# Kernel optimization log

Measured on AMD Instinct MI355X. Metric: run time of the kernel, lower is better.

## Reference

```python
import jax, jax.numpy as jnp
import numpy as np

N_KERNELS = 21
N_LAYERS = 2
N_HEADS = 8
ATT_DIM = 32
FF_HID = 100
EMB = 300


def kernel_mus(n):
    mus = [1.0]
    bin_size = 2.0 / (n - 1)
    mus.append(1.0 - bin_size / 2.0)
    for _ in range(1, n - 1):
        mus.append(mus[-1] - bin_size)
    return np.array(mus, dtype=np.float32)


def kernel_sigmas(n):
    return np.array([0.001] + [0.1] * (n - 1), dtype=np.float32)


def setup_inputs() -> dict:
    key = jax.random.key(0)
    ks = jax.random.split(key, 12)
    B, LQ, LD = 32, 64, 512
    u = lambda k, s, a: jax.random.uniform(k, s, jnp.float32, -a, a)
    return dict(
        q_embed=jax.random.normal(ks[0], (B, LQ, EMB), jnp.float32),
        d_embed=jax.random.normal(ks[1], (B, LD, EMB), jnp.float32),
        mask_q=(jax.random.uniform(ks[2], (B, LQ)) > 0.1).astype(jnp.float32),
        mask_d=(jax.random.uniform(ks[3], (B, LD)) > 0.1).astype(jnp.float32),
        mixer=jnp.full((1, 1, 1), 0.5, jnp.float32),
        nn_scaler=jnp.full((1,), 0.01, jnp.float32),
        ff_w1=u(ks[4], (N_LAYERS, EMB, FF_HID), 0.05),
        ff_b1=jnp.zeros((N_LAYERS, FF_HID), jnp.float32),
        ff_w2=u(ks[5], (N_LAYERS, FF_HID, EMB), 0.05),
        ff_b2=jnp.zeros((N_LAYERS, EMB), jnp.float32),
        ln1_g=jnp.ones((N_LAYERS, EMB), jnp.float32),
        ln1_b=jnp.zeros((N_LAYERS, EMB), jnp.float32),
        att_w=u(ks[6], (N_LAYERS, EMB, 3 * ATT_DIM), 0.05),
        att_b=jnp.zeros((N_LAYERS, 3 * ATT_DIM), jnp.float32),
        out_w=u(ks[7], (N_LAYERS, ATT_DIM, EMB), 0.05),
        out_b=jnp.zeros((N_LAYERS, EMB), jnp.float32),
        ln2_g=jnp.ones((N_LAYERS, EMB), jnp.float32),
        ln2_b=jnp.zeros((N_LAYERS, EMB), jnp.float32),
        dense_w=u(ks[8], (1, N_KERNELS), 0.014),
    )


def _layer_norm(x, g, b, eps=1e-6):
    m = jnp.mean(x, -1, keepdims=True)
    s = jnp.std(x, -1, keepdims=True, ddof=1)  # torch std is unbiased
    return g * (x - m) / (s + eps) + b


def _encoder(x, mask, p):
    # AllenNLP StackedSelfAttentionEncoder: [FF -> res+LN -> MHSA -> res+LN] x2
    B, T, E = x.shape
    scale = jnp.sqrt(jnp.float32(E // N_HEADS))
    hd = ATT_DIM // N_HEADS
    for l in range(N_LAYERS):
        h = jax.nn.relu(x @ p['ff_w1'][l] + p['ff_b1'][l]) @ p['ff_w2'][l] + p['ff_b2'][l]
        h = _layer_norm(h + x, p['ln1_g'][l], p['ln1_b'][l])
        c = h @ p['att_w'][l] + p['att_b'][l]              # [B,T,3*ATT_DIM]
        q = c[..., :ATT_DIM].reshape(B, T, N_HEADS, hd)
        k = c[..., ATT_DIM:2 * ATT_DIM].reshape(B, T, N_HEADS, hd)
        v = c[..., 2 * ATT_DIM:].reshape(B, T, N_HEADS, hd)
        sims = jnp.einsum('bqhd,bkhd->bhqk', q / scale, k)
        m = mask[:, None, None, :]
        att = jax.nn.softmax(sims * m, axis=-1) * m         # AllenNLP masked_softmax
        att = att / (jnp.sum(att, -1, keepdims=True) + 1e-13)
        o = jnp.einsum('bhqk,bkhd->bqhd', att, v).reshape(B, T, ATT_DIM)
        o = o @ p['out_w'][l] + p['out_b'][l]
        x = _layer_norm(o + h, p['ln2_g'][l], p['ln2_b'][l])
    return x


def reference(q_embed, d_embed, mask_q, mask_d, mixer, nn_scaler,
              ff_w1, ff_b1, ff_w2, ff_b2, ln1_g, ln1_b,
              att_w, att_b, out_w, out_b, ln2_g, ln2_b, dense_w):
    p = dict(ff_w1=ff_w1, ff_b1=ff_b1, ff_w2=ff_w2, ff_b2=ff_b2,
             ln1_g=ln1_g, ln1_b=ln1_b, att_w=att_w, att_b=att_b,
             out_w=out_w, out_b=out_b, ln2_g=ln2_g, ln2_b=ln2_b)
    mu = jnp.asarray(kernel_mus(N_KERNELS))        # [K]
    sigma = jnp.asarray(kernel_sigmas(N_KERNELS))  # [K]
    mq = mask_q[..., None]
    md = mask_d[..., None]
    q = q_embed * mq
    d = d_embed * md
    qc = _encoder(q, mask_q, p)
    dc = _encoder(d, mask_d, p)
    q = (mixer * q + (1.0 - mixer) * qc) * mq
    d = (mixer * d + (1.0 - mixer) * dc) * md
    qd_mask = mask_q[:, :, None] * mask_d[:, None, :]  # [B,Q,D]
    qn = q / (jnp.linalg.norm(q, axis=-1, keepdims=True) + 1e-13)
    dn = d / (jnp.linalg.norm(d, axis=-1, keepdims=True) + 1e-13)
    cos = jnp.einsum('bqe,bde->bqd', qn, dn) * qd_mask
    # Gaussian RBF soft histogram: [B,Q,D,K]
    kr = jnp.exp(-(cos[..., None] - mu) ** 2 / (2.0 * sigma ** 2)) * qd_mask[..., None]
    pkq = jnp.sum(kr, axis=2)                                 # [B,Q,K]
    log_pkq = jnp.log2(jnp.clip(pkq, 1e-10)) * nn_scaler
    per_kernel = jnp.sum(log_pkq * mq, axis=1)                # [B,K]
    return jnp.squeeze(per_kernel @ dense_w.T, axis=1)        # [B]
```

## Files before the change

kernel.cpp:

```cpp
#include <hip/hip_runtime.h>
#include <hip/hip_bf16.h>

#define BATCH 32
#define LQ 64
#define LD 512
#define EMB 300
#define FFH 100
#define ATTD 32
#define NH 8
#define NK 21
#define MQ (BATCH * LQ)
#define MD (BATCH * LD)
#define MALL (MQ + MD)

typedef __attribute__((ext_vector_type(8))) short bf16x8;
typedef __attribute__((ext_vector_type(4))) float f32x4;

__device__ __forceinline__ float wave_sum(float v) {
    #pragma unroll
    for (int off = 32; off > 0; off >>= 1) v += __shfl_xor(v, off);
    return v;
}

__device__ __forceinline__ float bf2f(__hip_bfloat16 h) {
    return __bfloat162float(h);
}

__device__ __forceinline__ float4 bf4_to_f4(const __hip_bfloat16* p) {
    uint2 u = *(const uint2*)p;
    float4 f;
    f.x = __uint_as_float((u.x & 0xffffu) << 16);
    f.y = __uint_as_float(u.x & 0xffff0000u);
    f.z = __uint_as_float((u.y & 0xffffu) << 16);
    f.w = __uint_as_float(u.y & 0xffff0000u);
    return f;
}

__global__ void maskmul_all(const float* __restrict__ q_embed, const float* __restrict__ d_embed,
                            const float* __restrict__ mask_q, const float* __restrict__ mask_d,
                            __hip_bfloat16* __restrict__ xbf, float* __restrict__ mall) {
    int i = blockIdx.x * blockDim.x + threadIdx.x;
    if (i >= MALL * EMB) return;
    int tok = i / EMB;
    float m, v;
    if (tok < MQ) {
        m = mask_q[tok];
        v = q_embed[i];
    } else {
        m = mask_d[tok - MQ];
        v = d_embed[i - MQ * EMB];
    }
    xbf[i] = __float2bfloat16(v * m);
    if (i % EMB == 0) mall[tok] = m;
}

__device__ __forceinline__ void conv_seg(const float* __restrict__ w, __hip_bfloat16* __restrict__ wt,
                                         int j, int K, int N) {
    int l = j / (K * N);
    int r = j % (K * N);
    int k = r / N, n = r % N;
    wt[(size_t)l * N * K + (size_t)n * K + k] = __float2bfloat16(w[j]);
}
__global__ void convert_all(const float* __restrict__ w1, const float* __restrict__ w2,
                            const float* __restrict__ aw, const float* __restrict__ ow,
                            __hip_bfloat16* __restrict__ w1t, __hip_bfloat16* __restrict__ w2t,
                            __hip_bfloat16* __restrict__ awt, __hip_bfloat16* __restrict__ owt) {
    int i = blockIdx.x * blockDim.x + threadIdx.x;
    const int S1 = 2 * EMB * FFH;
    const int S2 = S1 + 2 * 320 * 128;
    const int S3 = S2 + 2 * EMB * 96;
    const int S4 = S3 + 2 * 320 * 32;
    if (i < S1) {
        conv_seg(w1, w1t, i, EMB, FFH);
    } else if (i < S2) {
        int j = i - S1;
        int l = j / (320 * 128);
        int r = j % (320 * 128);
        int n = r / 128, k = r % 128;
        float v = (n < EMB && k < FFH) ? w2[(size_t)l * FFH * EMB + (size_t)k * EMB + n] : 0.f;
        w2t[j] = __float2bfloat16(v);
    } else if (i < S3) {
        conv_seg(aw, awt, i - S2, EMB, 96);
    } else if (i < S4) {
        int j = i - S3;
        int l = j / (320 * 32);
        int r = j % (320 * 32);
        int n = r / 32, k = r % 32;
        float v = (n < EMB && k < ATTD) ? ow[(size_t)l * ATTD * EMB + (size_t)k * EMB + n] : 0.f;
        owt[j] = __float2bfloat16(v);
    }
}

__device__ __forceinline__ void stage_row8(const __hip_bfloat16* __restrict__ src, bool rowvalid,
                                           int K, int gk, __hip_bfloat16* dst) {
    if (rowvalid && gk + 8 <= K) {
        const uint2* p = (const uint2*)(src + gk);
        uint2 a = p[0], b = p[1];
        *(uint2*)dst = a;
        *(uint2*)(dst + 4) = b;
    } else {
        #pragma unroll
        for (int j = 0; j < 8; j++)
            dst[j] = (rowvalid && gk + j < K) ? src[gk + j] : __float2bfloat16(0.f);
    }
}

template <bool RELU>
__global__ __launch_bounds__(256) void gemm_mfma(const __hip_bfloat16* __restrict__ A,
                                                 const __hip_bfloat16* __restrict__ Bt,
                                                 const float* __restrict__ bias,
                                                 __hip_bfloat16* __restrict__ Cb,
                                                 int M, int Nr, int Ns, int K) {
    __shared__ __align__(16) __hip_bfloat16 As[64][40];
    __shared__ __align__(16) __hip_bfloat16 Bs[64][40];
    const int tid = threadIdx.x;
    const int m0 = blockIdx.y * 64, n0 = blockIdx.x * 64;
    const int lane = tid & 63;
    const int wv = tid >> 6;
    const int wm = wv >> 1, wn = wv & 1;
    const int l15 = lane & 15, lg = lane >> 4;
    const int srow = tid >> 2, sk8 = (tid & 3) * 8;
    f32x4 acc[2][2] = {};
    const int NS = (K + 31) >> 5;
    const __hip_bfloat16* arow = A + (size_t)(m0 + srow) * K;
    const bool bvalid = (n0 + srow) < Nr;
    const __hip_bfloat16* brow = Bt + (size_t)(n0 + srow) * K;

    for (int s = 0; s < NS; s++) {
        const int gk = (s << 5) + sk8;
        if (s) __syncthreads();
        stage_row8(arow, true, K, gk, &As[srow][sk8]);
        stage_row8(brow, bvalid, K, gk, &Bs[srow][sk8]);
        __syncthreads();
        bf16x8 af0 = *(const bf16x8*)&As[wm * 32 + l15][lg * 8];
        bf16x8 af1 = *(const bf16x8*)&As[wm * 32 + 16 + l15][lg * 8];
        bf16x8 bf0 = *(const bf16x8*)&Bs[wn * 32 + l15][lg * 8];
        bf16x8 bf1 = *(const bf16x8*)&Bs[wn * 32 + 16 + l15][lg * 8];
        acc[0][0] = __builtin_amdgcn_mfma_f32_16x16x32_bf16(af0, bf0, acc[0][0], 0, 0, 0);
        acc[0][1] = __builtin_amdgcn_mfma_f32_16x16x32_bf16(af0, bf1, acc[0][1], 0, 0, 0);
        acc[1][0] = __builtin_amdgcn_mfma_f32_16x16x32_bf16(af1, bf0, acc[1][0], 0, 0, 0);
        acc[1][1] = __builtin_amdgcn_mfma_f32_16x16x32_bf16(af1, bf1, acc[1][1], 0, 0, 0);
    }

    #pragma unroll
    for (int fc = 0; fc < 2; fc++) {
        int col = n0 + wn * 32 + fc * 16 + l15;
        if (col >= Ns) continue;
        float bs = (col < Nr) ? bias[col] : 0.f;
        #pragma unroll
        for (int fr = 0; fr < 2; fr++) {
            int rbase = m0 + wm * 32 + fr * 16 + lg * 4;
            #pragma unroll
            for (int r = 0; r < 4; r++) {
                float v = acc[fr][fc][r] + bs;
                if (RELU) v = fmaxf(v, 0.f);
                Cb[(size_t)(rbase + r) * Ns + col] = __float2bfloat16(v);
            }
        }
    }
}

template <int NSTEP, int KSTR, int ASTR>
__global__ __launch_bounds__(256) void gemm_ln_direct(const __hip_bfloat16* __restrict__ A,
                                                      const __hip_bfloat16* __restrict__ Bt,
                                                      const float* __restrict__ bias,
                                                      const __hip_bfloat16* __restrict__ Res,
                                                      const float* __restrict__ g,
                                                      const float* __restrict__ beta,
                                                      __hip_bfloat16* __restrict__ Y) {
    const int tid = threadIdx.x;
    const int wv = tid >> 6;
    const int lane = tid & 63;
    const int l15 = lane & 15, lg = lane >> 4;
    const int m0 = blockIdx.x * 64 + wv * 16;

    f32x4 acc[19];
    #pragma unroll
    for (int fc = 0; fc < 19; fc++) acc[fc] = (f32x4){0.f, 0.f, 0.f, 0.f};

    #pragma unroll
    for (int ks = 0; ks < NSTEP; ks++) {
        const int kb = ks * 32 + lg * 8;
        bf16x8 af = *(const bf16x8*)(A + (size_t)(m0 + l15) * ASTR + kb);
        #pragma unroll
        for (int fc = 0; fc < 19; fc++) {
            bf16x8 bf = *(const bf16x8*)(Bt + (size_t)(fc * 16 + l15) * KSTR + kb);
            acc[fc] = __builtin_amdgcn_mfma_f32_16x16x32_bf16(af, bf, acc[fc], 0, 0, 0);
        }
    }

    float rs[4] = {0.f, 0.f, 0.f, 0.f};
    #pragma unroll
    for (int fc = 0; fc < 19; fc++) {
        int col = fc * 16 + l15;
        bool valid = col < EMB;
        float bs = valid ? bias[col] : 0.f;
        #pragma unroll
        for (int r = 0; r < 4; r++) {
            float v = 0.f;
            if (valid) v = acc[fc][r] + bs + bf2f(Res[(size_t)(m0 + lg * 4 + r) * EMB + col]);
            acc[fc][r] = v;
            rs[r] += v;
        }
    }
    #pragma unroll
    for (int r = 0; r < 4; r++)
        #pragma unroll
        for (int off = 1; off < 16; off <<= 1)
            rs[r] += __shfl_xor(rs[r], off);
    float mean[4], invv[4];
    #pragma unroll
    for (int r = 0; r < 4; r++) mean[r] = rs[r] * (1.f / EMB);

    float rq[4] = {0.f, 0.f, 0.f, 0.f};
    #pragma unroll
    for (int fc = 0; fc < 19; fc++) {
        int col = fc * 16 + l15;
        if (col < EMB) {
            #pragma unroll
            for (int r = 0; r < 4; r++) {
                float d = acc[fc][r] - mean[r];
                rq[r] += d * d;
            }
        }
    }
    #pragma unroll
    for (int r = 0; r < 4; r++) {
        #pragma unroll
        for (int off = 1; off < 16; off <<= 1)
            rq[r] += __shfl_xor(rq[r], off);
        float stdv = sqrtf(rq[r] * (1.f / (EMB - 1)));
        invv[r] = 1.f / (stdv + 1e-6f);
    }
    #pragma unroll
    for (int fc = 0; fc < 19; fc++) {
        int col = fc * 16 + l15;
        if (col >= EMB) continue;
        float gv = g[col], bv = beta[col];
        #pragma unroll
        for (int r = 0; r < 4; r++) {
            float y = gv * (acc[fc][r] - mean[r]) * invv[r] + bv;
            Y[(size_t)(m0 + lg * 4 + r) * EMB + col] = __float2bfloat16(y);
        }
    }
}

__global__ __launch_bounds__(256) void cos_mfma(const __hip_bfloat16* __restrict__ Qn,
                                                const __hip_bfloat16* __restrict__ Dn,
                                                float* __restrict__ Cos) {
    __shared__ __align__(16) __hip_bfloat16 As[64][40];
    __shared__ __align__(16) __hip_bfloat16 Bs[64][40];
    const int b = blockIdx.y;
    const int n0 = blockIdx.x * 64;
    const int tid = threadIdx.x;
    const int lane = tid & 63;
    const int wv = tid >> 6;
    const int wm = wv >> 1, wn = wv & 1;
    const int l15 = lane & 15, lg = lane >> 4;
    const int srow = tid >> 2, sk8 = (tid & 3) * 8;
    f32x4 acc[2][2] = {};
    const int NS = (EMB + 31) >> 5;
    const __hip_bfloat16* arow = Qn + ((size_t)b * LQ + srow) * EMB;
    const __hip_bfloat16* brow = Dn + ((size_t)b * LD + n0 + srow) * EMB;

    for (int s = 0; s < NS; s++) {
        const int gk = (s << 5) + sk8;
        if (s) __syncthreads();
        stage_row8(arow, true, EMB, gk, &As[srow][sk8]);
        stage_row8(brow, true, EMB, gk, &Bs[srow][sk8]);
        __syncthreads();
        bf16x8 af0 = *(const bf16x8*)&As[wm * 32 + l15][lg * 8];
        bf16x8 af1 = *(const bf16x8*)&As[wm * 32 + 16 + l15][lg * 8];
        bf16x8 bf0 = *(const bf16x8*)&Bs[wn * 32 + l15][lg * 8];
        bf16x8 bf1 = *(const bf16x8*)&Bs[wn * 32 + 16 + l15][lg * 8];
        acc[0][0] = __builtin_amdgcn_mfma_f32_16x16x32_bf16(af0, bf0, acc[0][0], 0, 0, 0);
        acc[0][1] = __builtin_amdgcn_mfma_f32_16x16x32_bf16(af0, bf1, acc[0][1], 0, 0, 0);
        acc[1][0] = __builtin_amdgcn_mfma_f32_16x16x32_bf16(af1, bf0, acc[1][0], 0, 0, 0);
        acc[1][1] = __builtin_amdgcn_mfma_f32_16x16x32_bf16(af1, bf1, acc[1][1], 0, 0, 0);
    }

    float* cb = Cos + (size_t)b * LQ * LD;
    #pragma unroll
    for (int fc = 0; fc < 2; fc++) {
        int col = n0 + wn * 32 + fc * 16 + l15;
        #pragma unroll
        for (int fr = 0; fr < 2; fr++) {
            int rbase = wm * 32 + fr * 16 + lg * 4;
            #pragma unroll
            for (int r = 0; r < 4; r++) {
                cb[(size_t)(rbase + r) * LD + col] = acc[fr][fc][r];
            }
        }
    }
}

template <int T, int RPB, int KS>
__device__ __forceinline__ void attn_body(const __hip_bfloat16* __restrict__ cseg,
                                          const float* __restrict__ mask,
                                          __hip_bfloat16* __restrict__ oseg,
                                          int bh, int rb, char* smem) {
    constexpr int BLK = 512;
    float4* Ks = (float4*)smem;
    float4* Vs = Ks + T;
    float* part = (float*)(Vs + T);
    float* nmask_s = part + RPB * 5 * (KS - 1);
    const int b = bh / NH, h = bh % NH;
    const int tid = threadIdx.x;
    const __hip_bfloat16* base = cseg + (size_t)b * T * 96;

    if (tid == 0) *nmask_s = 0.f;
    __syncthreads();
    float lnm = 0.f;
    for (int j = tid; j < T; j += BLK) {
        float m = mask[b * T + j];
        float4 kv = bf4_to_f4(base + (size_t)j * 96 + ATTD + h * 4);
        float4 vv = bf4_to_f4(base + (size_t)j * 96 + 2 * ATTD + h * 4);
        kv.x *= m; kv.y *= m; kv.z *= m; kv.w *= m;
        vv.x *= m; vv.y *= m; vv.z *= m; vv.w *= m;
        Ks[j] = kv;
        Vs[j] = vv;
        lnm += 1.f - m;
    }
    lnm = wave_sum(lnm);
    if ((tid & 63) == 0 && lnm != 0.f) atomicAdd(nmask_s, lnm);
    __syncthreads();

    const int r = rb * RPB + (tid % RPB);
    const int ks = tid / RPB;
    const float inv_scale = 0.16439898730535729f;
    float4 qv = bf4_to_f4(base + (size_t)r * 96 + h * 4);
    qv.x *= inv_scale; qv.y *= inv_scale; qv.z *= inv_scale; qv.w *= inv_scale;

    float Sall = 0.f, ox = 0.f, oy = 0.f, oz = 0.f, ow = 0.f;
    constexpr int KC = T / KS;
    const int k0 = ks * KC;
    #pragma unroll 4
    for (int k = k0; k < k0 + KC; k++) {
        float4 kv = Ks[k];
        float4 vv = Vs[k];
        float s = fmaf(qv.x, kv.x, fmaf(qv.y, kv.y, fmaf(qv.z, kv.z, qv.w * kv.w)));
        float e = __expf(s);
        Sall += e;
        ox = fmaf(e, vv.x, ox);
        oy = fmaf(e, vv.y, oy);
        oz = fmaf(e, vv.z, oz);
        ow = fmaf(e, vv.w, ow);
    }
    if (ks > 0) {
        float* p = &part[((ks - 1) * RPB + (tid % RPB)) * 5];
        p[0] = Sall; p[1] = ox; p[2] = oy; p[3] = oz; p[4] = ow;
    }
    __syncthreads();
    if (ks == 0) {
        #pragma unroll
        for (int s2 = 0; s2 < KS - 1; s2++) {
            const float* p = &part[(s2 * RPB + r - rb * RPB) * 5];
            Sall += p[0]; ox += p[1]; oy += p[2]; oz += p[3]; ow += p[4];
        }
        float Sm = Sall - *nmask_s;
        float inv = 1.f / (Sm + 1e-13f * Sall);
        __hip_bfloat16* op = oseg + (size_t)(b * T + r) * ATTD + h * 4;
        op[0] = __float2bfloat16(ox * inv);
        op[1] = __float2bfloat16(oy * inv);
        op[2] = __float2bfloat16(oz * inv);
        op[3] = __float2bfloat16(ow * inv);
    }
}

__global__ __launch_bounds__(512) void attn_both(const __hip_bfloat16* __restrict__ cbf,
                                                 const float* __restrict__ mask_q,
                                                 const float* __restrict__ mask_d,
                                                 __hip_bfloat16* __restrict__ o32) {
    __shared__ __align__(16) char smem[24576];
    int blk = blockIdx.x;
    if (blk < BATCH * NH) {
        attn_body<LQ, 64, 8>(cbf, mask_q, o32, blk, 0, smem);
    } else {
        int bid = blk - BATCH * NH;
        attn_body<LD, 128, 4>(cbf + (size_t)MQ * 96, mask_d, o32 + (size_t)MQ * ATTD,
                              bid >> 2, bid & 3, smem);
    }
}

__global__ __launch_bounds__(256) void mixnorm_bf(const __hip_bfloat16* __restrict__ x,
                                                  const __hip_bfloat16* __restrict__ xc,
                                                  const float* __restrict__ mask,
                                                  const float* __restrict__ mixer,
                                                  __hip_bfloat16* __restrict__ out) {
    int wid = (blockIdx.x * 256 + threadIdx.x) >> 6;
    int lane = threadIdx.x & 63;
    float mixv = mixer[0];
    float mval = mask[wid];
    const __hip_bfloat16* xr = x + (size_t)wid * EMB;
    const __hip_bfloat16* xcr = xc + (size_t)wid * EMB;
    float v[5];
    float s2 = 0.f;
    #pragma unroll
    for (int r = 0; r < 5; r++) {
        int idx = lane + r * 64;
        float val = 0.f;
        if (idx < EMB) val = (mixv * bf2f(xr[idx]) + (1.f - mixv) * bf2f(xcr[idx])) * mval;
        v[r] = val;
        s2 += val * val;
    }
    s2 = wave_sum(s2);
    float inv = 1.f / (sqrtf(s2) + 1e-13f);
    __hip_bfloat16* o = out + (size_t)wid * EMB;
    #pragma unroll
    for (int r = 0; r < 5; r++) {
        int idx = lane + r * 64;
        if (idx < EMB) o[idx] = __float2bfloat16(v[r] * inv);
    }
}

__global__ __launch_bounds__(256) void pool_kernel(const float* __restrict__ Cos,
                                                   const float* __restrict__ mask_q,
                                                   const float* __restrict__ mask_d,
                                                   const float* __restrict__ nn_scaler,
                                                   float* __restrict__ lp) {
    int wid = (blockIdx.x * 256 + threadIdx.x) >> 6;
    int lane = threadIdx.x & 63;
    int b = wid >> 6, qi = wid & 63;
    const float* crow = Cos + ((size_t)b * LQ + qi) * LD;
    const float* md = mask_d + b * LD;
    float acc[NK];
    #pragma unroll
    for (int k = 0; k < NK; k++) acc[k] = 0.f;
    #pragma unroll
    for (int rr = 0; rr < LD / 64; rr++) {
        int dj = rr * 64 + lane;
        float m = md[dj];
        if (m != 0.f) {
            float cv = crow[dj];
            float d0 = cv - 1.0f;
            acc[0] += __expf(d0 * d0 * -500000.0f);
            #pragma unroll
            for (int g = 0; g < 4; g++) {
                float mu_a = 0.95f - 0.5f * g;
                float dc = cv - mu_a;
                float t = __expf(dc * dc * -50.0f);
                float r = __expf(fmaf(-10.0f, dc, -0.5f));
                #pragma unroll
                for (int j = 0; j < 5; j++) {
                    acc[1 + 5 * g + j] += t;
                    t *= r;
                    r *= 0.36787944117144233f;
                }
            }
        }
    }
    float mq = mask_q[b * LQ + qi];
    float ns = nn_scaler[0];
    #pragma unroll
    for (int k = 0; k < NK; k++) {
        float s = wave_sum(acc[k]);
        if (lane == 0) lp[((size_t)b * LQ + qi) * NK + k] = log2f(fmaxf(s, 1e-10f)) * ns * mq;
    }
}

__global__ void final_kernel(const float* __restrict__ lp, const float* __restrict__ dense_w,
                             float* __restrict__ out) {
    int b = blockIdx.x;
    int t = threadIdx.x;
    float s = 0.f;
    if (t < NK) {
        for (int qi = 0; qi < LQ; qi++) s += lp[((size_t)b * LQ + qi) * NK + t];
        s *= dense_w[t];
    }
    s = wave_sum(s);
    if (t == 0) out[b] = s;
}

extern "C" void kernel_launch(void* const* d_in, const int* in_sizes, int n_in,
                              void* d_out, int out_size, void* d_ws, size_t ws_size,
                              hipStream_t stream) {
    (void)in_sizes; (void)n_in; (void)out_size; (void)ws_size;
    const float* q_embed  = (const float*)d_in[0];
    const float* d_embed  = (const float*)d_in[1];
    const float* mask_q   = (const float*)d_in[2];
    const float* mask_d   = (const float*)d_in[3];
    const float* mixer    = (const float*)d_in[4];
    const float* nn_scaler= (const float*)d_in[5];
    const float* ff_w1    = (const float*)d_in[6];
    const float* ff_b1    = (const float*)d_in[7];
    const float* ff_w2    = (const float*)d_in[8];
    const float* ff_b2    = (const float*)d_in[9];
    const float* ln1_g    = (const float*)d_in[10];
    const float* ln1_b    = (const float*)d_in[11];
    const float* att_w    = (const float*)d_in[12];
    const float* att_b    = (const float*)d_in[13];
    const float* out_w    = (const float*)d_in[14];
    const float* out_b    = (const float*)d_in[15];
    const float* ln2_g    = (const float*)d_in[16];
    const float* ln2_b    = (const float*)d_in[17];
    const float* dense_w  = (const float*)d_in[18];
    float* out = (float*)d_out;

    float* ws   = (float*)d_ws;
    float* cosb = ws;
    float* lp   = cosb + 1048576;
    float* mall = lp + 43008;
    __hip_bfloat16* xbf   = (__hip_bfloat16*)(mall + MALL);
    __hip_bfloat16* xcbf  = xbf  + (size_t)MALL * EMB;
    __hip_bfloat16* xc2bf = xcbf + (size_t)MALL * EMB;
    __hip_bfloat16* hbf   = xc2bf + (size_t)MALL * EMB;
    __hip_bfloat16* t1bf  = hbf  + (size_t)MALL * EMB;
    __hip_bfloat16* cbf   = t1bf + (size_t)MALL * 128;
    __hip_bfloat16* o32bf = cbf  + (size_t)MALL * 96;
    __hip_bfloat16* w1t   = o32bf + (size_t)MALL * ATTD;
    __hip_bfloat16* w2t   = w1t + 2 * FFH * EMB;
    __hip_bfloat16* awt   = w2t + 2 * 320 * 128;
    __hip_bfloat16* owt   = awt + 2 * 96 * EMB;

    convert_all<<<(220000 + 255) / 256, 256, 0, stream>>>(ff_w1, ff_w2, att_w, out_w,
                                                          w1t, w2t, awt, owt);
    maskmul_all<<<(MALL * EMB + 255) / 256, 256, 0, stream>>>(q_embed, d_embed, mask_q, mask_d,
                                                              xbf, mall);

    const __hip_bfloat16* xcur = xbf;
    for (int l = 0; l < 2; l++) {
        __hip_bfloat16* xout = (l == 0) ? xcbf : xc2bf;
        gemm_mfma<true><<<dim3(2, MALL / 64), 256, 0, stream>>>(
            xcur, w1t + (size_t)l * FFH * EMB, ff_b1 + l * FFH, t1bf, MALL, FFH, 128, EMB);
        gemm_ln_direct<4, 128, 128><<<MALL / 64, 256, 0, stream>>>(
            t1bf, w2t + (size_t)l * 320 * 128, ff_b2 + l * EMB, xcur,
            ln1_g + l * EMB, ln1_b + l * EMB, hbf);
        gemm_mfma<false><<<dim3(2, MALL / 64), 256, 0, stream>>>(
            hbf, awt + (size_t)l * 96 * EMB, att_b + l * 96, cbf, MALL, 96, 96, EMB);
        attn_both<<<BATCH * NH + BATCH * NH * (LD / 128), 512, 0, stream>>>(
            cbf, mask_q, mask_d, o32bf);
        gemm_ln_direct<1, 32, 32><<<MALL / 64, 256, 0, stream>>>(
            o32bf, owt + (size_t)l * 320 * 32, out_b + l * EMB, hbf,
            ln2_g + l * EMB, ln2_b + l * EMB, xout);
        xcur = xout;
    }

    mixnorm_bf<<<MALL / 4, 256, 0, stream>>>(xbf, xc2bf, mall, mixer, hbf);

    cos_mfma<<<dim3(LD / 64, BATCH), 256, 0, stream>>>(hbf, hbf + (size_t)MQ * EMB, cosb);

    pool_kernel<<<(BATCH * LQ) / 4, 256, 0, stream>>>(cosb, mask_q, mask_d, nn_scaler, lp);

    final_kernel<<<BATCH, 64, 0, stream>>>(lp, dense_w, out);
}
```

Measured before the change: 243.0 us.

## Fuse RBF kernel pooling into cosine MFMA epilogue with atomic accumulation

The cosine-similarity GEMM now computes the Gaussian RBF soft histogram directly in its epilogue. It reduces across lanes and atomically adds per-query kernel sums into a buffer that is zeroed in the weight conversion kernel. This removes the 4 MB cosine matrix write and read and the separate pool kernel, and moves the log2, mask and scaling into the final kernel. mixnorm is also vectorized to 4-wide bf16 loads and stores. The cost is extra shuffle reductions and atomics per tile in the GEMM epilogue, plus nondeterministic float summation order.

```diff
diff --git a/kernel.cpp b/kernel.cpp
--- a/kernel.cpp
+++ b/kernel.cpp
@@ -34,6 +34,11 @@
     f.z = __uint_as_float((u.y & 0xffffu) << 16);
     f.w = __uint_as_float(u.y & 0xffff0000u);
     return f;
+}
+
+__device__ __forceinline__ unsigned short f2bfu(float x) {
+    __hip_bfloat16 h = __float2bfloat16(x);
+    return *(unsigned short*)&h;
 }
 
 __global__ void maskmul_all(const float* __restrict__ q_embed, const float* __restrict__ d_embed,
@@ -64,12 +69,14 @@
 __global__ void convert_all(const float* __restrict__ w1, const float* __restrict__ w2,
                             const float* __restrict__ aw, const float* __restrict__ ow,
                             __hip_bfloat16* __restrict__ w1t, __hip_bfloat16* __restrict__ w2t,
-                            __hip_bfloat16* __restrict__ awt, __hip_bfloat16* __restrict__ owt) {
+                            __hip_bfloat16* __restrict__ awt, __hip_bfloat16* __restrict__ owt,
+                            float* __restrict__ lpraw) {
     int i = blockIdx.x * blockDim.x + threadIdx.x;
     const int S1 = 2 * EMB * FFH;
     const int S2 = S1 + 2 * 320 * 128;
     const int S3 = S2 + 2 * EMB * 96;
     const int S4 = S3 + 2 * 320 * 32;
+    const int S5 = S4 + BATCH * LQ * NK;
     if (i < S1) {
         conv_seg(w1, w1t, i, EMB, FFH);
     } else if (i < S2) {
@@ -88,6 +95,8 @@
         int n = r / 32, k = r % 32;
         float v = (n < EMB && k < ATTD) ? ow[(size_t)l * ATTD * EMB + (size_t)k * EMB + n] : 0.f;
         owt[j] = __float2bfloat16(v);
+    } else if (i < S5) {
+        lpraw[i - S4] = 0.f;
     }
 }
 
@@ -245,9 +254,28 @@
     }
 }
 
-__global__ __launch_bounds__(256) void cos_mfma(const __hip_bfloat16* __restrict__ Qn,
-                                                const __hip_bfloat16* __restrict__ Dn,
-                                                float* __restrict__ Cos) {
+__device__ __forceinline__ void rbf_acc(float cv, float* ks) {
+    float d0 = cv - 1.0f;
+    ks[0] += __expf(d0 * d0 * -500000.0f);
+    #pragma unroll
+    for (int g = 0; g < 4; g++) {
+        float mu_a = 0.95f - 0.5f * g;
+        float dc = cv - mu_a;
+        float t = __expf(dc * dc * -50.0f);
+        float r = __expf(fmaf(-10.0f, dc, -0.5f));
+        #pragma unroll
+        for (int j = 0; j < 5; j++) {
+            ks[1 + 5 * g + j] += t;
+            t *= r;
+            r *= 0.36787944117144233f;
+        }
+    }
+}
+
+__global__ __launch_bounds__(256) void cos_pool_mfma(const __hip_bfloat16* __restrict__ Qn,
+                                                     const __hip_bfloat16* __restrict__ Dn,
+                                                     const float* __restrict__ mask_d,
+                                                     float* __restrict__ lpraw) {
     __shared__ __align__(16) __hip_bfloat16 As[64][40];
     __shared__ __align__(16) __hip_bfloat16 Bs[64][40];
     const int b = blockIdx.y;
@@ -279,16 +307,30 @@
         acc[1][1] = __builtin_amdgcn_mfma_f32_16x16x32_bf16(af1, bf1, acc[1][1], 0, 0, 0);
     }
 
-    float* cb = Cos + (size_t)b * LQ * LD;
-    #pragma unroll
-    for (int fc = 0; fc < 2; fc++) {
-        int col = n0 + wn * 32 + fc * 16 + l15;
-        #pragma unroll
-        for (int fr = 0; fr < 2; fr++) {
-            int rbase = wm * 32 + fr * 16 + lg * 4;
+    const float* md = mask_d + b * LD;
+    float mc0 = md[n0 + wn * 32 + l15];
+    float mc1 = md[n0 + wn * 32 + 16 + l15];
+
+    #pragma unroll
+    for (int fr = 0; fr < 2; fr++) {
+        #pragma unroll
+        for (int r = 0; r < 4; r++) {
+            int qrow = wm * 32 + fr * 16 + lg * 4 + r;
+            float ks[NK];
             #pragma unroll
-            for (int r = 0; r < 4; r++) {
-                cb[(size_t)(rbase + r) * LD + col] = acc[fr][fc][r];
+            for (int k = 0; k < NK; k++) ks[k] = 0.f;
+            if (mc0 != 0.f) rbf_acc(acc[fr][0][r], ks);
+            if (mc1 != 0.f) rbf_acc(acc[fr][1][r], ks);
+            #pragma unroll
+            for (int k = 0; k < NK; k++) {
+                #pragma unroll
+                for (int off = 1; off < 16; off <<= 1)
+                    ks[k] += __shfl_xor(ks[k], off);
+            }
+            if (l15 == 0) {
+                float* dst = lpraw + ((size_t)b * LQ + qrow) * NK;
+                #pragma unroll
+                for (int k = 0; k < NK; k++) atomicAdd(&dst[k], ks[k]);
             }
         }
     }
@@ -393,79 +435,58 @@
     float mval = mask[wid];
     const __hip_bfloat16* xr = x + (size_t)wid * EMB;
     const __hip_bfloat16* xcr = xc + (size_t)wid * EMB;
-    float v[5];
+    const bool hasB = lane < 11;
+    float vA[4], vB[4];
     float s2 = 0.f;
-    #pragma unroll
-    for (int r = 0; r < 5; r++) {
-        int idx = lane + r * 64;
-        float val = 0.f;
-        if (idx < EMB) val = (mixv * bf2f(xr[idx]) + (1.f - mixv) * bf2f(xcr[idx])) * mval;
-        v[r] = val;
-        s2 += val * val;
+    {
+        float4 xa = bf4_to_f4(xr + lane * 4);
+        float4 xca = bf4_to_f4(xcr + lane * 4);
+        vA[0] = (mixv * xa.x + (1.f - mixv) * xca.x) * mval;
+        vA[1] = (mixv * xa.y + (1.f - mixv) * xca.y) * mval;
+        vA[2] = (mixv * xa.z + (1.f - mixv) * xca.z) * mval;
+        vA[3] = (mixv * xa.w + (1.f - mixv) * xca.w) * mval;
+        s2 += vA[0] * vA[0] + vA[1] * vA[1] + vA[2] * vA[2] + vA[3] * vA[3];
+    }
+    if (hasB) {
+        int c = 64 + lane;
+        float4 xa = bf4_to_f4(xr + c * 4);
+        float4 xca = bf4_to_f4(xcr + c * 4);
+        vB[0] = (mixv * xa.x + (1.f - mixv) * xca.x) * mval;
+        vB[1] = (mixv * xa.y + (1.f - mixv) * xca.y) * mval;
+        vB[2] = (mixv * xa.z + (1.f - mixv) * xca.z) * mval;
+        vB[3] = (mixv * xa.w + (1.f - mixv) * xca.w) * mval;
+        s2 += vB[0] * vB[0] + vB[1] * vB[1] + vB[2] * vB[2] + vB[3] * vB[3];
     }
     s2 = wave_sum(s2);
     float inv = 1.f / (sqrtf(s2) + 1e-13f);
     __hip_bfloat16* o = out + (size_t)wid * EMB;
-    #pragma unroll
-    for (int r = 0; r < 5; r++) {
-        int idx = lane + r * 64;
-        if (idx < EMB) o[idx] = __float2bfloat16(v[r] * inv);
-    }
-}
-
-__global__ __launch_bounds__(256) void pool_kernel(const float* __restrict__ Cos,
-                                                   const float* __restrict__ mask_q,
-                                                   const float* __restrict__ mask_d,
-                                                   const float* __restrict__ nn_scaler,
-                                                   float* __restrict__ lp) {
-    int wid = (blockIdx.x * 256 + threadIdx.x) >> 6;
-    int lane = threadIdx.x & 63;
-    int b = wid >> 6, qi = wid & 63;
-    const float* crow = Cos + ((size_t)b * LQ + qi) * LD;
-    const float* md = mask_d + b * LD;
-    float acc[NK];
-    #pragma unroll
-    for (int k = 0; k < NK; k++) acc[k] = 0.f;
-    #pragma unroll
-    for (int rr = 0; rr < LD / 64; rr++) {
-        int dj = rr * 64 + lane;
-        float m = md[dj];
-        if (m != 0.f) {
-            float cv = crow[dj];
-            float d0 = cv - 1.0f;
-            acc[0] += __expf(d0 * d0 * -500000.0f);
-            #pragma unroll
-            for (int g = 0; g < 4; g++) {
-                float mu_a = 0.95f - 0.5f * g;
-                float dc = cv - mu_a;
-                float t = __expf(dc * dc * -50.0f);
-                float r = __expf(fmaf(-10.0f, dc, -0.5f));
-                #pragma unroll
-                for (int j = 0; j < 5; j++) {
-                    acc[1 + 5 * g + j] += t;
-                    t *= r;
-                    r *= 0.36787944117144233f;
-                }
-            }
-        }
-    }
-    float mq = mask_q[b * LQ + qi];
-    float ns = nn_scaler[0];
-    #pragma unroll
-    for (int k = 0; k < NK; k++) {
-        float s = wave_sum(acc[k]);
-        if (lane == 0) lp[((size_t)b * LQ + qi) * NK + k] = log2f(fmaxf(s, 1e-10f)) * ns * mq;
-    }
-}
-
-__global__ void final_kernel(const float* __restrict__ lp, const float* __restrict__ dense_w,
+    {
+        uint2 u;
+        u.x = (unsigned)f2bfu(vA[0] * inv) | ((unsigned)f2bfu(vA[1] * inv) << 16);
+        u.y = (unsigned)f2bfu(vA[2] * inv) | ((unsigned)f2bfu(vA[3] * inv) << 16);
+        *(uint2*)(o + lane * 4) = u;
+    }
+    if (hasB) {
+        int c = 64 + lane;
+        uint2 u;
+        u.x = (unsigned)f2bfu(vB[0] * inv) | ((unsigned)f2bfu(vB[1] * inv) << 16);
+        u.y = (unsigned)f2bfu(vB[2] * inv) | ((unsigned)f2bfu(vB[3] * inv) << 16);
+        *(uint2*)(o + c * 4) = u;
+    }
+}
+
+__global__ void final_kernel(const float* __restrict__ lpraw, const float* __restrict__ mask_q,
+                             const float* __restrict__ nn_scaler, const float* __restrict__ dense_w,
                              float* __restrict__ out) {
     int b = blockIdx.x;
     int t = threadIdx.x;
     float s = 0.f;
     if (t < NK) {
-        for (int qi = 0; qi < LQ; qi++) s += lp[((size_t)b * LQ + qi) * NK + t];
-        s *= dense_w[t];
+        for (int qi = 0; qi < LQ; qi++) {
+            float pkq = lpraw[((size_t)b * LQ + qi) * NK + t];
+            s += log2f(fmaxf(pkq, 1e-10f)) * mask_q[b * LQ + qi];
+        }
+        s *= nn_scaler[0] * dense_w[t];
     }
     s = wave_sum(s);
     if (t == 0) out[b] = s;
@@ -496,10 +517,9 @@
     const float* dense_w  = (const float*)d_in[18];
     float* out = (float*)d_out;
 
-    float* ws   = (float*)d_ws;
-    float* cosb = ws;
-    float* lp   = cosb + 1048576;
-    float* mall = lp + 43008;
+    float* ws    = (float*)d_ws;
+    float* lpraw = ws;
+    float* mall  = lpraw + 43008;
     __hip_bfloat16* xbf   = (__hip_bfloat16*)(mall + MALL);
     __hip_bfloat16* xcbf  = xbf  + (size_t)MALL * EMB;
     __hip_bfloat16* xc2bf = xcbf + (size_t)MALL * EMB;
@@ -512,8 +532,8 @@
     __hip_bfloat16* awt   = w2t + 2 * 320 * 128;
     __hip_bfloat16* owt   = awt + 2 * 96 * EMB;
 
-    convert_all<<<(220000 + 255) / 256, 256, 0, stream>>>(ff_w1, ff_w2, att_w, out_w,
-                                                          w1t, w2t, awt, owt);
+    convert_all<<<(263008 + 255) / 256, 256, 0, stream>>>(ff_w1, ff_w2, att_w, out_w,
+                                                          w1t, w2t, awt, owt, lpraw);
     maskmul_all<<<(MALL * EMB + 255) / 256, 256, 0, stream>>>(q_embed, d_embed, mask_q, mask_d,
                                                               xbf, mall);
 
@@ -537,9 +557,8 @@
 
     mixnorm_bf<<<MALL / 4, 256, 0, stream>>>(xbf, xc2bf, mall, mixer, hbf);
 
-    cos_mfma<<<dim3(LD / 64, BATCH), 256, 0, stream>>>(hbf, hbf + (size_t)MQ * EMB, cosb);
-
-    pool_kernel<<<(BATCH * LQ) / 4, 256, 0, stream>>>(cosb, mask_q, mask_d, nn_scaler, lp);
-
-    final_kernel<<<BATCH, 64, 0, stream>>>(lp, dense_w, out);
-}
+    cos_pool_mfma<<<dim3(LD / 64, BATCH), 256, 0, stream>>>(
+        hbf, hbf + (size_t)MQ * EMB, mask_d, lpraw);
+
+    final_kernel<<<BATCH, 64, 0, stream>>>(lpraw, mask_q, nn_scaler, dense_w, out);
+}
```

After: 291.8 us. +20.1%, slower.

## Fuse FF1, FF2+LN and QKV GEMMs into one encoder kernel with padded stride

Applied to the files above, without the earlier changes.

Replaces three per-layer launches (FF1 GEMM, FF2 GEMM with LayerNorm, QKV GEMM) with one kernel per 64-row tile. The ReLU hidden activations and the normalized rows now stay in shared memory instead of going through global buffers. Activations are stored at a padded row stride of 320, and the weight-convert and mask kernels are merged into a single prep launch. The mix-and-normalize kernel is also vectorized to 4-element bf16 loads and stores. The risk is that the padded columns 300–319 of the activation buffers are never written, so the fused GEMM reads uninitialized bf16 values there and relies on the zero-padded weights to cancel them.

```diff
diff --git a/kernel.cpp b/kernel.cpp
--- a/kernel.cpp
+++ b/kernel.cpp
@@ -12,6 +12,7 @@
 #define MQ (BATCH * LQ)
 #define MD (BATCH * LD)
 #define MALL (MQ + MD)
+#define STR 320
 
 typedef __attribute__((ext_vector_type(8))) short bf16x8;
 typedef __attribute__((ext_vector_type(4))) float f32x4;
@@ -22,9 +23,7 @@
     return v;
 }
 
-__device__ __forceinline__ float bf2f(__hip_bfloat16 h) {
-    return __bfloat162float(h);
-}
+__device__ __forceinline__ float bf2f(__hip_bfloat16 h) { return __bfloat162float(h); }
 
 __device__ __forceinline__ float4 bf4_to_f4(const __hip_bfloat16* p) {
     uint2 u = *(const uint2*)p;
@@ -36,57 +35,58 @@
     return f;
 }
 
-__global__ void maskmul_all(const float* __restrict__ q_embed, const float* __restrict__ d_embed,
-                            const float* __restrict__ mask_q, const float* __restrict__ mask_d,
-                            __hip_bfloat16* __restrict__ xbf, float* __restrict__ mall) {
+__device__ __forceinline__ unsigned short f2bfu(float x) {
+    __hip_bfloat16 h = __float2bfloat16(x);
+    return *(unsigned short*)&h;
+}
+
+__global__ void prep_all(const float* __restrict__ qe, const float* __restrict__ de,
+                         const float* __restrict__ mq, const float* __restrict__ md,
+                         const float* __restrict__ w1, const float* __restrict__ w2,
+                         const float* __restrict__ aw, const float* __restrict__ ow,
+                         __hip_bfloat16* __restrict__ xbf, float* __restrict__ mall,
+                         __hip_bfloat16* __restrict__ w1t, __hip_bfloat16* __restrict__ w2t,
+                         __hip_bfloat16* __restrict__ awt, __hip_bfloat16* __restrict__ owt) {
     int i = blockIdx.x * blockDim.x + threadIdx.x;
-    if (i >= MALL * EMB) return;
-    int tok = i / EMB;
-    float m, v;
-    if (tok < MQ) {
-        m = mask_q[tok];
-        v = q_embed[i];
-    } else {
-        m = mask_d[tok - MQ];
-        v = d_embed[i - MQ * EMB];
-    }
-    xbf[i] = __float2bfloat16(v * m);
-    if (i % EMB == 0) mall[tok] = m;
-}
-
-__device__ __forceinline__ void conv_seg(const float* __restrict__ w, __hip_bfloat16* __restrict__ wt,
-                                         int j, int K, int N) {
-    int l = j / (K * N);
-    int r = j % (K * N);
-    int k = r / N, n = r % N;
-    wt[(size_t)l * N * K + (size_t)n * K + k] = __float2bfloat16(w[j]);
-}
-__global__ void convert_all(const float* __restrict__ w1, const float* __restrict__ w2,
-                            const float* __restrict__ aw, const float* __restrict__ ow,
-                            __hip_bfloat16* __restrict__ w1t, __hip_bfloat16* __restrict__ w2t,
-                            __hip_bfloat16* __restrict__ awt, __hip_bfloat16* __restrict__ owt) {
-    int i = blockIdx.x * blockDim.x + threadIdx.x;
-    const int S1 = 2 * EMB * FFH;
-    const int S2 = S1 + 2 * 320 * 128;
-    const int S3 = S2 + 2 * EMB * 96;
-    const int S4 = S3 + 2 * 320 * 32;
-    if (i < S1) {
-        conv_seg(w1, w1t, i, EMB, FFH);
-    } else if (i < S2) {
-        int j = i - S1;
-        int l = j / (320 * 128);
-        int r = j % (320 * 128);
+    const int NM = MALL * EMB;
+    if (i < NM) {
+        int tok = i / EMB, c = i % EMB;
+        float m, v;
+        if (tok < MQ) { m = mq[tok]; v = qe[i]; }
+        else          { m = md[tok - MQ]; v = de[i - MQ * EMB]; }
+        xbf[(size_t)tok * STR + c] = __float2bfloat16(v * m);
+        if (c == 0) mall[tok] = m;
+        return;
+    }
+    int j = i - NM;
+    if (j < 2 * 112 * 320) {
+        int l = j / (112 * 320), r = j % (112 * 320);
+        int n = r / 320, k = r % 320;
+        float v = (n < FFH && k < EMB) ? w1[(size_t)l * EMB * FFH + (size_t)k * FFH + n] : 0.f;
+        w1t[j] = __float2bfloat16(v);
+        return;
+    }
+    j -= 2 * 112 * 320;
+    if (j < 2 * 304 * 128) {
+        int l = j / (304 * 128), r = j % (304 * 128);
         int n = r / 128, k = r % 128;
         float v = (n < EMB && k < FFH) ? w2[(size_t)l * FFH * EMB + (size_t)k * EMB + n] : 0.f;
         w2t[j] = __float2bfloat16(v);
-    } else if (i < S3) {
-        conv_seg(aw, awt, i - S2, EMB, 96);
-    } else if (i < S4) {
-        int j = i - S3;
-        int l = j / (320 * 32);
-        int r = j % (320 * 32);
+        return;
+    }
+    j -= 2 * 304 * 128;
+    if (j < 2 * 96 * 320) {
+        int l = j / (96 * 320), r = j % (96 * 320);
+        int n = r / 320, k = r % 320;
+        float v = (k < EMB) ? aw[(size_t)l * EMB * 96 + (size_t)k * 96 + n] : 0.f;
+        awt[j] = __float2bfloat16(v);
+        return;
+    }
+    j -= 2 * 96 * 320;
+    if (j < 2 * 304 * 32) {
+        int l = j / (304 * 32), r = j % (304 * 32);
         int n = r / 32, k = r % 32;
-        float v = (n < EMB && k < ATTD) ? ow[(size_t)l * ATTD * EMB + (size_t)k * EMB + n] : 0.f;
+        float v = (n < EMB) ? ow[(size_t)l * ATTD * EMB + (size_t)k * EMB + n] : 0.f;
         owt[j] = __float2bfloat16(v);
     }
 }
@@ -105,62 +105,162 @@
     }
 }
 
-template <bool RELU>
-__global__ __launch_bounds__(256) void gemm_mfma(const __hip_bfloat16* __restrict__ A,
-                                                 const __hip_bfloat16* __restrict__ Bt,
-                                                 const float* __restrict__ bias,
-                                                 __hip_bfloat16* __restrict__ Cb,
-                                                 int M, int Nr, int Ns, int K) {
-    __shared__ __align__(16) __hip_bfloat16 As[64][40];
-    __shared__ __align__(16) __hip_bfloat16 Bs[64][40];
+__global__ __launch_bounds__(256) void enc_fused(const __hip_bfloat16* __restrict__ X,
+                                                 const __hip_bfloat16* __restrict__ W1t,
+                                                 const float* __restrict__ b1,
+                                                 const __hip_bfloat16* __restrict__ W2t,
+                                                 const float* __restrict__ b2,
+                                                 const float* __restrict__ g1,
+                                                 const float* __restrict__ bt1,
+                                                 const __hip_bfloat16* __restrict__ AWt,
+                                                 const float* __restrict__ ab,
+                                                 __hip_bfloat16* __restrict__ Hout,
+                                                 __hip_bfloat16* __restrict__ Cout) {
+    __shared__ __align__(16) __hip_bfloat16 t1s[64][136];
+    __shared__ __align__(16) __hip_bfloat16 hs[64][328];
     const int tid = threadIdx.x;
-    const int m0 = blockIdx.y * 64, n0 = blockIdx.x * 64;
-    const int lane = tid & 63;
-    const int wv = tid >> 6;
-    const int wm = wv >> 1, wn = wv & 1;
+    const int wv = tid >> 6, lane = tid & 63;
     const int l15 = lane & 15, lg = lane >> 4;
-    const int srow = tid >> 2, sk8 = (tid & 3) * 8;
-    f32x4 acc[2][2] = {};
-    const int NS = (K + 31) >> 5;
-    const __hip_bfloat16* arow = A + (size_t)(m0 + srow) * K;
-    const bool bvalid = (n0 + srow) < Nr;
-    const __hip_bfloat16* brow = Bt + (size_t)(n0 + srow) * K;
-
-    for (int s = 0; s < NS; s++) {
-        const int gk = (s << 5) + sk8;
-        if (s) __syncthreads();
-        stage_row8(arow, true, K, gk, &As[srow][sk8]);
-        stage_row8(brow, bvalid, K, gk, &Bs[srow][sk8]);
-        __syncthreads();
-        bf16x8 af0 = *(const bf16x8*)&As[wm * 32 + l15][lg * 8];
-        bf16x8 af1 = *(const bf16x8*)&As[wm * 32 + 16 + l15][lg * 8];
-        bf16x8 bf0 = *(const bf16x8*)&Bs[wn * 32 + l15][lg * 8];
-        bf16x8 bf1 = *(const bf16x8*)&Bs[wn * 32 + 16 + l15][lg * 8];
-        acc[0][0] = __builtin_amdgcn_mfma_f32_16x16x32_bf16(af0, bf0, acc[0][0], 0, 0, 0);
-        acc[0][1] = __builtin_amdgcn_mfma_f32_16x16x32_bf16(af0, bf1, acc[0][1], 0, 0, 0);
-        acc[1][0] = __builtin_amdgcn_mfma_f32_16x16x32_bf16(af1, bf0, acc[1][0], 0, 0, 0);
-        acc[1][1] = __builtin_amdgcn_mfma_f32_16x16x32_bf16(af1, bf1, acc[1][1], 0, 0, 0);
-    }
-
-    #pragma unroll
-    for (int fc = 0; fc < 2; fc++) {
-        int col = n0 + wn * 32 + fc * 16 + l15;
-        if (col >= Ns) continue;
-        float bs = (col < Nr) ? bias[col] : 0.f;
-        #pragma unroll
-        for (int fr = 0; fr < 2; fr++) {
-            int rbase = m0 + wm * 32 + fr * 16 + lg * 4;
+    const int m0 = blockIdx.x * 64;
+    const int rw = wv * 16;
+
+    {
+        int rr = tid >> 2, cc = (tid & 3) * 4;
+        *(uint2*)&t1s[rr][112 + cc] = (uint2){0u, 0u};
+        *(uint2*)&hs[rr][304 + cc] = (uint2){0u, 0u};
+    }
+
+    {
+        f32x4 a1[7];
+        #pragma unroll
+        for (int fc = 0; fc < 7; fc++) a1[fc] = (f32x4){0.f, 0.f, 0.f, 0.f};
+        #pragma unroll
+        for (int ks = 0; ks < 10; ks++) {
+            const int kb = ks * 32 + lg * 8;
+            bf16x8 af = *(const bf16x8*)(X + (size_t)(m0 + rw + l15) * STR + kb);
+            #pragma unroll
+            for (int fc = 0; fc < 7; fc++) {
+                bf16x8 bf = *(const bf16x8*)(W1t + (size_t)(fc * 16 + l15) * STR + kb);
+                a1[fc] = __builtin_amdgcn_mfma_f32_16x16x32_bf16(af, bf, a1[fc], 0, 0, 0);
+            }
+        }
+        #pragma unroll
+        for (int fc = 0; fc < 7; fc++) {
+            int col = fc * 16 + l15;
+            float bs = (col < FFH) ? b1[col] : 0.f;
             #pragma unroll
             for (int r = 0; r < 4; r++) {
-                float v = acc[fr][fc][r] + bs;
-                if (RELU) v = fmaxf(v, 0.f);
-                Cb[(size_t)(rbase + r) * Ns + col] = __float2bfloat16(v);
-            }
-        }
-    }
-}
-
-template <int NSTEP, int KSTR, int ASTR>
+                float v = fmaxf(a1[fc][r] + bs, 0.f);
+                t1s[rw + lg * 4 + r][col] = __float2bfloat16(v);
+            }
+        }
+    }
+    __syncthreads();
+
+    {
+        f32x4 a2[19];
+        #pragma unroll
+        for (int fc = 0; fc < 19; fc++) a2[fc] = (f32x4){0.f, 0.f, 0.f, 0.f};
+        #pragma unroll
+        for (int ks = 0; ks < 4; ks++) {
+            const int kb = ks * 32 + lg * 8;
+            bf16x8 af = *(const bf16x8*)&t1s[rw + l15][kb];
+            #pragma unroll
+            for (int fc = 0; fc < 19; fc++) {
+                bf16x8 bf = *(const bf16x8*)(W2t + (size_t)(fc * 16 + l15) * 128 + kb);
+                a2[fc] = __builtin_amdgcn_mfma_f32_16x16x32_bf16(af, bf, a2[fc], 0, 0, 0);
+            }
+        }
+        float rs[4] = {0.f, 0.f, 0.f, 0.f};
+        #pragma unroll
+        for (int fc = 0; fc < 19; fc++) {
+            int col = fc * 16 + l15;
+            bool valid = col < EMB;
+            float bs = valid ? b2[col] : 0.f;
+            #pragma unroll
+            for (int r = 0; r < 4; r++) {
+                float v = 0.f;
+                if (valid) v = a2[fc][r] + bs + bf2f(X[(size_t)(m0 + rw + lg * 4 + r) * STR + col]);
+                a2[fc][r] = v;
+                rs[r] += v;
+            }
+        }
+        #pragma unroll
+        for (int r = 0; r < 4; r++)
+            #pragma unroll
+            for (int off = 1; off < 16; off <<= 1)
+                rs[r] += __shfl_xor(rs[r], off);
+        float mean[4], invv[4];
+        #pragma unroll
+        for (int r = 0; r < 4; r++) mean[r] = rs[r] * (1.f / EMB);
+        float rq[4] = {0.f, 0.f, 0.f, 0.f};
+        #pragma unroll
+        for (int fc = 0; fc < 19; fc++) {
+            int col = fc * 16 + l15;
+            if (col < EMB) {
+                #pragma unroll
+                for (int r = 0; r < 4; r++) {
+                    float d = a2[fc][r] - mean[r];
+                    rq[r] += d * d;
+                }
+            }
+        }
+        #pragma unroll
+        for (int r = 0; r < 4; r++) {
+            #pragma unroll
+            for (int off = 1; off < 16; off <<= 1)
+                rq[r] += __shfl_xor(rq[r], off);
+            float stdv = sqrtf(rq[r] * (1.f / (EMB - 1)));
+            invv[r] = 1.f / (stdv + 1e-6f);
+        }
+        #pragma unroll
+        for (int fc = 0; fc < 19; fc++) {
+            int col = fc * 16 + l15;
+            if (col < EMB) {
+                float gv = g1[col], bv = bt1[col];
+                #pragma unroll
+                for (int r = 0; r < 4; r++) {
+                    int row = rw + lg * 4 + r;
+                    float y = gv * (a2[fc][r] - mean[r]) * invv[r] + bv;
+                    __hip_bfloat16 yb = __float2bfloat16(y);
+                    hs[row][col] = yb;
+                    Hout[(size_t)(m0 + row) * STR + col] = yb;
+                }
+            } else {
+                #pragma unroll
+                for (int r = 0; r < 4; r++) hs[rw + lg * 4 + r][col] = __float2bfloat16(0.f);
+            }
+        }
+    }
+    __syncthreads();
+
+    {
+        f32x4 a3[6];
+        #pragma unroll
+        for (int fc = 0; fc < 6; fc++) a3[fc] = (f32x4){0.f, 0.f, 0.f, 0.f};
+        #pragma unroll
+        for (int ks = 0; ks < 10; ks++) {
+            const int kb = ks * 32 + lg * 8;
+            bf16x8 af = *(const bf16x8*)&hs[rw + l15][kb];
+            #pragma unroll
+            for (int fc = 0; fc < 6; fc++) {
+                bf16x8 bf = *(const bf16x8*)(AWt + (size_t)(fc * 16 + l15) * STR + kb);
+                a3[fc] = __builtin_amdgcn_mfma_f32_16x16x32_bf16(af, bf, a3[fc], 0, 0, 0);
+            }
+        }
+        #pragma unroll
+        for (int fc = 0; fc < 6; fc++) {
+            int col = fc * 16 + l15;
+            float bs = ab[col];
+            #pragma unroll
+            for (int r = 0; r < 4; r++)
+                Cout[(size_t)(m0 + rw + lg * 4 + r) * 96 + col] =
+                    __float2bfloat16(a3[fc][r] + bs);
+        }
+    }
+}
+
+template <int NSTEP, int KSTR, int ASTR, int RSTR>
 __global__ __launch_bounds__(256) void gemm_ln_direct(const __hip_bfloat16* __restrict__ A,
                                                       const __hip_bfloat16* __restrict__ Bt,
                                                       const float* __restrict__ bias,
@@ -198,7 +298,7 @@
         #pragma unroll
         for (int r = 0; r < 4; r++) {
             float v = 0.f;
-            if (valid) v = acc[fc][r] + bs + bf2f(Res[(size_t)(m0 + lg * 4 + r) * EMB + col]);
+            if (valid) v = acc[fc][r] + bs + bf2f(Res[(size_t)(m0 + lg * 4 + r) * RSTR + col]);
             acc[fc][r] = v;
             rs[r] += v;
         }
@@ -240,7 +340,7 @@
         #pragma unroll
         for (int r = 0; r < 4; r++) {
             float y = gv * (acc[fc][r] - mean[r]) * invv[r] + bv;
-            Y[(size_t)(m0 + lg * 4 + r) * EMB + col] = __float2bfloat16(y);
+            Y[(size_t)(m0 + lg * 4 + r) * RSTR + col] = __float2bfloat16(y);
         }
     }
 }
@@ -260,8 +360,8 @@
     const int srow = tid >> 2, sk8 = (tid & 3) * 8;
     f32x4 acc[2][2] = {};
     const int NS = (EMB + 31) >> 5;
-    const __hip_bfloat16* arow = Qn + ((size_t)b * LQ + srow) * EMB;
-    const __hip_bfloat16* brow = Dn + ((size_t)b * LD + n0 + srow) * EMB;
+    const __hip_bfloat16* arow = Qn + (size_t)(b * LQ + srow) * STR;
+    const __hip_bfloat16* brow = Dn + (size_t)(b * LD + n0 + srow) * STR;
 
     for (int s = 0; s < NS; s++) {
         const int gk = (s << 5) + sk8;
@@ -391,25 +491,45 @@
     int lane = threadIdx.x & 63;
     float mixv = mixer[0];
     float mval = mask[wid];
-    const __hip_bfloat16* xr = x + (size_t)wid * EMB;
-    const __hip_bfloat16* xcr = xc + (size_t)wid * EMB;
-    float v[5];
+    const __hip_bfloat16* xr = x + (size_t)wid * STR;
+    const __hip_bfloat16* xcr = xc + (size_t)wid * STR;
+    const bool hasB = lane < 11;
+    float vA[4], vB[4];
     float s2 = 0.f;
-    #pragma unroll
-    for (int r = 0; r < 5; r++) {
-        int idx = lane + r * 64;
-        float val = 0.f;
-        if (idx < EMB) val = (mixv * bf2f(xr[idx]) + (1.f - mixv) * bf2f(xcr[idx])) * mval;
-        v[r] = val;
-        s2 += val * val;
+    {
+        float4 xa = bf4_to_f4(xr + lane * 4);
+        float4 xca = bf4_to_f4(xcr + lane * 4);
+        vA[0] = (mixv * xa.x + (1.f - mixv) * xca.x) * mval;
+        vA[1] = (mixv * xa.y + (1.f - mixv) * xca.y) * mval;
+        vA[2] = (mixv * xa.z + (1.f - mixv) * xca.z) * mval;
+        vA[3] = (mixv * xa.w + (1.f - mixv) * xca.w) * mval;
+        s2 += vA[0] * vA[0] + vA[1] * vA[1] + vA[2] * vA[2] + vA[3] * vA[3];
+    }
+    if (hasB) {
+        int c = 64 + lane;
+        float4 xa = bf4_to_f4(xr + c * 4);
+        float4 xca = bf4_to_f4(xcr + c * 4);
+        vB[0] = (mixv * xa.x + (1.f - mixv) * xca.x) * mval;
+        vB[1] = (mixv * xa.y + (1.f - mixv) * xca.y) * mval;
+        vB[2] = (mixv * xa.z + (1.f - mixv) * xca.z) * mval;
+        vB[3] = (mixv * xa.w + (1.f - mixv) * xca.w) * mval;
+        s2 += vB[0] * vB[0] + vB[1] * vB[1] + vB[2] * vB[2] + vB[3] * vB[3];
     }
     s2 = wave_sum(s2);
     float inv = 1.f / (sqrtf(s2) + 1e-13f);
-    __hip_bfloat16* o = out + (size_t)wid * EMB;
-    #pragma unroll
-    for (int r = 0; r < 5; r++) {
-        int idx = lane + r * 64;
-        if (idx < EMB) o[idx] = __float2bfloat16(v[r] * inv);
+    __hip_bfloat16* o = out + (size_t)wid * STR;
+    {
+        uint2 u;
+        u.x = (unsigned)f2bfu(vA[0] * inv) | ((unsigned)f2bfu(vA[1] * inv) << 16);
+        u.y = (unsigned)f2bfu(vA[2] * inv) | ((unsigned)f2bfu(vA[3] * inv) << 16);
+        *(uint2*)(o + lane * 4) = u;
+    }
+    if (hasB) {
+        int c = 64 + lane;
+        uint2 u;
+        u.x = (unsigned)f2bfu(vB[0] * inv) | ((unsigned)f2bfu(vB[1] * inv) << 16);
+        u.y = (unsigned)f2bfu(vB[2] * inv) | ((unsigned)f2bfu(vB[3] * inv) << 16);
+        *(uint2*)(o + c * 4) = u;
     }
 }
 
@@ -501,43 +621,42 @@
     float* lp   = cosb + 1048576;
     float* mall = lp + 43008;
     __hip_bfloat16* xbf   = (__hip_bfloat16*)(mall + MALL);
-    __hip_bfloat16* xcbf  = xbf  + (size_t)MALL * EMB;
-    __hip_bfloat16* xc2bf = xcbf + (size_t)MALL * EMB;
-    __hip_bfloat16* hbf   = xc2bf + (size_t)MALL * EMB;
-    __hip_bfloat16* t1bf  = hbf  + (size_t)MALL * EMB;
-    __hip_bfloat16* cbf   = t1bf + (size_t)MALL * 128;
+    __hip_bfloat16* xcbf  = xbf  + (size_t)MALL * STR;
+    __hip_bfloat16* xc2bf = xcbf + (size_t)MALL * STR;
+    __hip_bfloat16* hbf   = xc2bf + (size_t)MALL * STR;
+    __hip_bfloat16* cbf   = hbf  + (size_t)MALL * STR;
     __hip_bfloat16* o32bf = cbf  + (size_t)MALL * 96;
     __hip_bfloat16* w1t   = o32bf + (size_t)MALL * ATTD;
-    __hip_bfloat16* w2t   = w1t + 2 * FFH * EMB;
-    __hip_bfloat16* awt   = w2t + 2 * 320 * 128;
-    __hip_bfloat16* owt   = awt + 2 * 96 * EMB;
-
-    convert_all<<<(220000 + 255) / 256, 256, 0, stream>>>(ff_w1, ff_w2, att_w, out_w,
-                                                          w1t, w2t, awt, owt);
-    maskmul_all<<<(MALL * EMB + 255) / 256, 256, 0, stream>>>(q_embed, d_embed, mask_q, mask_d,
-                                                              xbf, mall);
+    __hip_bfloat16* w2t   = w1t + 2 * 112 * 320;
+    __hip_bfloat16* awt   = w2t + 2 * 304 * 128;
+    __hip_bfloat16* owt   = awt + 2 * 96 * 320;
+
+    const int PREP_N = MALL * EMB + 2 * 112 * 320 + 2 * 304 * 128 + 2 * 96 * 320 + 2 * 304 * 32;
+    prep_all<<<(PREP_N + 255) / 256, 256, 0, stream>>>(
+        q_embed, d_embed, mask_q, mask_d, ff_w1, ff_w2, att_w, out_w,
+        xbf, mall, w1t, w2t, awt, owt);
 
     const __hip_bfloat16* xcur = xbf;
     for (int l = 0; l < 2; l++) {
         __hip_bfloat16* xout = (l == 0) ? xcbf : xc2bf;
-        gemm_mfma<true><<<dim3(2, MALL / 64), 256, 0, stream>>>(
-            xcur, w1t + (size_t)l * FFH * EMB, ff_b1 + l * FFH, t1bf, MALL, FFH, 128, EMB);
-        gemm_ln_direct<4, 128, 128><<<MALL / 64, 256, 0, stream>>>(
-            t1bf, w2t + (size_t)l * 320 * 128, ff_b2 + l * EMB, xcur,
-            ln1_g + l * EMB, ln1_b + l * EMB, hbf);
-        gemm_mfma<false><<<dim3(2, MALL / 64), 256, 0, stream>>>(
-            hbf, awt + (size_t)l * 96 * EMB, att_b + l * 96, cbf, MALL, 96, 96, EMB);
+        enc_fused<<<MALL / 64, 256, 0, stream>>>(
+            xcur,
+            w1t + (size_t)l * 112 * 320, ff_b1 + l * FFH,
+            w2t + (size_t)l * 304 * 128, ff_b2 + l * EMB,
+            ln1_g + l * EMB, ln1_b + l * EMB,
+            awt + (size_t)l * 96 * 320, att_b + l * 96,
+            hbf, cbf);
         attn_both<<<BATCH * NH + BATCH * NH * (LD / 128), 512, 0, stream>>>(
             cbf, mask_q, mask_d, o32bf);
-        gemm_ln_direct<1, 32, 32><<<MALL / 64, 256, 0, stream>>>(
-            o32bf, owt + (size_t)l * 320 * 32, out_b + l * EMB, hbf,
+        gemm_ln_direct<1, 32, 32, STR><<<MALL / 64, 256, 0, stream>>>(
+            o32bf, owt + (size_t)l * 304 * 32, out_b + l * EMB, hbf,
             ln2_g + l * EMB, ln2_b + l * EMB, xout);
         xcur = xout;
     }
 
     mixnorm_bf<<<MALL / 4, 256, 0, stream>>>(xbf, xc2bf, mall, mixer, hbf);
 
-    cos_mfma<<<dim3(LD / 64, BATCH), 256, 0, stream>>>(hbf, hbf + (size_t)MQ * EMB, cosb);
+    cos_mfma<<<dim3(LD / 64, BATCH), 256, 0, stream>>>(hbf, hbf + (size_t)MQ * STR, cosb);
 
     pool_kernel<<<(BATCH * LQ) / 4, 256, 0, stream>>>(cosb, mask_q, mask_d, nn_scaler, lp);
 
```

Measured after the change: 250.6 us. +3.1%, slower.
